# Kernel tuning notes

Measured on AMD Instinct MI355X. Metric: run time of the kernel, lower is better.

## Reference

```python
import jax, jax.numpy as jnp
import numpy as np

H = 1024
HEADS = 16
FFN = 2048
EPS = 1e-5


def _layernorm(x, g, b):
    mu = jnp.mean(x, axis=-1, keepdims=True)
    var = jnp.mean(jnp.square(x - mu), axis=-1, keepdims=True)
    return (x - mu) * jax.lax.rsqrt(var + EPS) * g + b


def setup_inputs() -> dict:
    key = jax.random.key(0)
    ks = jax.random.split(key, 8)
    N, L = 4, 1024
    s = 1.0 / np.sqrt(H)
    inp = {
        "src_hidden": jax.random.normal(ks[0], (N, L, H), dtype=jnp.float32),
        "src_mask": jnp.ones((N, L), dtype=jnp.int32),
        "Wq": jax.random.normal(ks[1], (H, H), dtype=jnp.float32) * s,
        "bq": jnp.zeros((H,), jnp.float32),
        "Wk": jax.random.normal(ks[2], (H, H), dtype=jnp.float32) * s,
        "bk": jnp.zeros((H,), jnp.float32),
        "Wv": jax.random.normal(ks[3], (H, H), dtype=jnp.float32) * s,
        "bv": jnp.zeros((H,), jnp.float32),
        "Wo": jax.random.normal(ks[4], (H, H), dtype=jnp.float32) * s,
        "bo": jnp.zeros((H,), jnp.float32),
        "ln1_g": jnp.ones((H,), jnp.float32),
        "ln1_b": jnp.zeros((H,), jnp.float32),
        "W1": jax.random.normal(ks[5], (H, FFN), dtype=jnp.float32) * s,
        "b1": jnp.zeros((FFN,), jnp.float32),
        "W2": jax.random.normal(ks[6], (FFN, H), dtype=jnp.float32) * (1.0 / np.sqrt(FFN)),
        "b2": jnp.zeros((H,), jnp.float32),
        "ln2_g": jnp.ones((H,), jnp.float32),
        "ln2_b": jnp.zeros((H,), jnp.float32),
    }
    return inp


def reference(src_hidden, src_mask, Wq, bq, Wk, bk, Wv, bv, Wo, bo,
              ln1_g, ln1_b, W1, b1, W2, b2, ln2_g, ln2_b):
    N, L, _ = src_hidden.shape
    d = H // HEADS
    scale = 1.0 / np.sqrt(H)  # applied to BOTH Q and K, as in the original
    # NOTE: head split is a plain reshape (view), faithful to the original code
    Q = ((src_hidden @ Wq + bq).reshape(N, HEADS, L, d)) * scale
    K = ((src_hidden @ Wk + bk).reshape(N, HEADS, L, d)) * scale
    V = (src_hidden @ Wv + bv).reshape(N, HEADS, L, d)
    sims = jnp.einsum('nhid,nhjd->nhij', Q, K)  # (N, heads, L, L)
    mask = src_mask[:, None, None, :]  # (N,1,1,L) broadcasts over heads and query dim
    sims = jnp.where(mask == 0, -jnp.inf, sims)
    attn = jax.nn.softmax(sims, axis=-1)
    ctx = jnp.einsum('nhij,nhjd->nhid', attn, V)
    concats = ctx.reshape(N, L, H)
    hid = concats @ Wo + bo
    x1 = _layernorm(hid, ln1_g, ln1_b) + hid
    ffn = jax.nn.relu(x1 @ W1 + b1) @ W2 + b2  # dropout is identity in eval
    out = _layernorm(ffn, ln2_g, ln2_b) + ffn
    return (out, src_mask)
```

## Files before the change

### kernel.cpp

```cpp
#include <hip/hip_runtime.h>
#include <math.h>

#define H 1024
#define HEADS 16
#define DH 64
#define FFN_DIM 2048
#define EPS 1e-5f
#define NB 4
#define LL 1024
#define M_ROWS 4096

typedef __attribute__((ext_vector_type(8))) short bf16x8;
typedef __attribute__((ext_vector_type(4))) float f32x4;

__device__ __forceinline__ ushort f2bf(float x) {
    union { float f; unsigned u; } c; c.f = x;
    unsigned u = c.u;
    u += 0x7FFFu + ((u >> 16) & 1u);
    return (ushort)(u >> 16);
}

__device__ __forceinline__ unsigned pack2bf(float a, float b) {
    union { float f; unsigned u; } ca, cb; ca.f = a; cb.f = b;
    const unsigned ua = ca.u + 0x8000u;
    const unsigned ub = cb.u + 0x8000u;
    return (ua >> 16) | (ub & 0xFFFF0000u);
}

#define GLL(gp, lp)                                                         \
    __builtin_amdgcn_global_load_lds(                                       \
        (const __attribute__((address_space(1))) void*)(gp),                \
        (__attribute__((address_space(3))) void*)(lp), 16, 0, 0)

#define WAITV4() asm volatile("s_waitcnt vmcnt(4)" ::: "memory")
#define WAITV2() asm volatile("s_waitcnt vmcnt(2)" ::: "memory")
#define WAITV0() asm volatile("s_waitcnt vmcnt(0)" ::: "memory")
#define BAR() __builtin_amdgcn_s_barrier()

__global__ __launch_bounds__(512, 8)
void gemm_bf16(const ushort* __restrict__ A, const ushort* __restrict__ Bt,
               const float* __restrict__ bias, float* __restrict__ Cf0,
               float* __restrict__ Cf1, ushort* __restrict__ Cb,
               int M, int N, int K, int relu, int qkv)
{
    __shared__ ushort As[2][128 * 32];
    __shared__ ushort Bs[2][128 * 32];
    const int tid = threadIdx.x;
    const int l = tid & 63, w = tid >> 6;
    const int wr = w >> 2, wc = w & 3;
    const int g = l >> 4, c0 = l & 15;
    const int brow = blockIdx.y * 128, bcol = blockIdx.x * 128;
    const int z = blockIdx.z;
    const int Ksub = K / gridDim.z;
    const int NS = Ksub >> 5;

    const ushort* Abase = A + (size_t)brow * K + (size_t)z * Ksub;
    const ushort* Bbase = Bt + (size_t)bcol * K + (size_t)z * Ksub;

    f32x4 acc[4][2];
    #pragma unroll
    for (int mi = 0; mi < 4; ++mi)
        #pragma unroll
        for (int ni = 0; ni < 2; ++ni)
            acc[mi][ni] = (f32x4)0.0f;

    auto stage = [&](int buf, int k0) {
        const int row = tid >> 2, cp = tid & 3;
        const int c = cp ^ ((row >> 1) & 3);
        const ushort* ga = Abase + (size_t)row * K + k0 + c * 8;
        const ushort* gb = Bbase + (size_t)row * K + k0 + c * 8;
        ushort* la = As[buf] + (size_t)w * 512;
        ushort* lb = Bs[buf] + (size_t)w * 512;
        GLL(ga, la);
        GLL(gb, lb);
    };

    stage(0, 0);
    int cur = 0;
    for (int t = 0; t < NS; ++t) {
        if (t + 1 < NS) { stage(cur ^ 1, (t + 1) << 5); WAITV2(); }
        else            { WAITV0(); }
        BAR();

        bf16x8 af[4], bf[2];
        #pragma unroll
        for (int mi = 0; mi < 4; ++mi) {
            const int row = wr * 64 + mi * 16 + c0;
            const int cc = g ^ ((row >> 1) & 3);
            af[mi] = *(const bf16x8*)&As[cur][row * 32 + cc * 8];
        }
        #pragma unroll
        for (int ni = 0; ni < 2; ++ni) {
            const int row = wc * 32 + ni * 16 + c0;
            const int cc = g ^ ((row >> 1) & 3);
            bf[ni] = *(const bf16x8*)&Bs[cur][row * 32 + cc * 8];
        }
        __builtin_amdgcn_s_setprio(1);
        #pragma unroll
        for (int mi = 0; mi < 4; ++mi)
            #pragma unroll
            for (int ni = 0; ni < 2; ++ni)
                acc[mi][ni] = __builtin_amdgcn_mfma_f32_16x16x32_bf16(
                    af[mi], bf[ni], acc[mi][ni], 0, 0, 0);
        __builtin_amdgcn_s_setprio(0);
        BAR();
        cur ^= 1;
    }

    float* Cf = (z == 0) ? Cf0 : Cf1;
    const int colg0 = bcol + wc * 32 + c0;
    const int rbase = brow + wr * 64 + (g << 2);
    const int seg   = qkv ? (bcol >> 10) : 0;
    const int Nw    = qkv ? 1024 : N;
    ushort* outb    = qkv ? (Cb + (size_t)seg * 4194304u) : Cb;
    #pragma unroll
    for (int ni = 0; ni < 2; ++ni) {
        const int colg = colg0 + ni * 16;
        const int colw = qkv ? (colg & 1023) : colg;
        const float bv = (z == 0) ? bias[colg] : 0.0f;
        #pragma unroll
        for (int mi = 0; mi < 4; ++mi) {
            #pragma unroll
            for (int j = 0; j < 4; ++j) {
                float v = acc[mi][ni][j] + bv;
                if (relu) v = fmaxf(v, 0.0f);
                const size_t off = (size_t)(rbase + mi * 16 + j) * Nw + colw;
                if (Cf) Cf[off] = v;
                if (Cb) outb[off] = f2bf(v);
            }
        }
    }
}

__global__ __launch_bounds__(256)
void transpose_qkvo(const float* __restrict__ Wq, const float* __restrict__ Wk,
                    const float* __restrict__ Wv, const float* __restrict__ Wo,
                    ushort* __restrict__ Dq, ushort* __restrict__ Dk,
                    ushort* __restrict__ Dv, ushort* __restrict__ Do_)
{
    const float* W; ushort* D; float sc;
    switch (blockIdx.z) {
        case 0:  W = Wq; D = Dq;  sc = 0.03125f; break;
        case 1:  W = Wk; D = Dk;  sc = 0.03125f; break;
        case 2:  W = Wv; D = Dv;  sc = 1.0f;     break;
        default: W = Wo; D = Do_; sc = 1.0f;     break;
    }
    __shared__ float t[32][33];
    const int n0 = blockIdx.x * 32, k0 = blockIdx.y * 32;
    const int tx = threadIdx.x & 31, ty = threadIdx.x >> 5;
    #pragma unroll
    for (int r = 0; r < 4; ++r)
        t[ty + r * 8][tx] = W[(size_t)(k0 + ty + r * 8) * H + n0 + tx];
    __syncthreads();
    #pragma unroll
    for (int r = 0; r < 4; ++r)
        D[(size_t)(n0 + ty + r * 8) * H + k0 + tx] =
            f2bf(t[tx][ty + r * 8] * sc);
}

__global__ __launch_bounds__(256)
void transpose_to_bf16(const float* __restrict__ W, ushort* __restrict__ Wt,
                       int K, int N, float scale)
{
    __shared__ float t[32][33];
    const int n0 = blockIdx.x * 32, k0 = blockIdx.y * 32;
    const int tx = threadIdx.x & 31, ty = threadIdx.x >> 5;
    #pragma unroll
    for (int r = 0; r < 4; ++r)
        t[ty + r * 8][tx] = W[(size_t)(k0 + ty + r * 8) * N + n0 + tx];
    __syncthreads();
    #pragma unroll
    for (int r = 0; r < 4; ++r)
        Wt[(size_t)(n0 + ty + r * 8) * K + k0 + tx] =
            f2bf(t[tx][ty + r * 8] * scale);
}

__global__ __launch_bounds__(256)
void transpose_v(const ushort* __restrict__ V, ushort* __restrict__ Vt)
{
    const int nh = blockIdx.y, jt = blockIdx.x;
    const size_t base = (size_t)nh << 16;
    __shared__ ushort t[64][68];
    const int tid = threadIdx.x;
    #pragma unroll
    for (int pass = 0; pass < 4; ++pass) {
        const int j = pass * 16 + (tid >> 4);
        const int d0 = (tid & 15) * 4;
        ushort4 v = *(const ushort4*)&V[base + (size_t)(jt * 64 + j) * 64 + d0];
        t[d0 + 0][j] = v.x; t[d0 + 1][j] = v.y;
        t[d0 + 2][j] = v.z; t[d0 + 3][j] = v.w;
    }
    __syncthreads();
    #pragma unroll
    for (int pass = 0; pass < 4; ++pass) {
        const int d = pass * 16 + (tid >> 4);
        const int j0 = (tid & 15) * 4;
        ushort4 o;
        o.x = t[d][j0 + 0]; o.y = t[d][j0 + 1];
        o.z = t[d][j0 + 2]; o.w = t[d][j0 + 3];
        *(ushort4*)&Vt[base + (size_t)d * 1024 + jt * 64 + j0] = o;
    }
}

__global__ __launch_bounds__(256)
void f32_to_bf16(const float* __restrict__ in, ushort* __restrict__ out, int n4)
{
    const int i = blockIdx.x * blockDim.x + threadIdx.x;
    if (i < n4) {
        float4 v = *reinterpret_cast<const float4*>(&in[i * 4]);
        ushort4 o;
        o.x = f2bf(v.x); o.y = f2bf(v.y); o.z = f2bf(v.z); o.w = f2bf(v.w);
        *reinterpret_cast<ushort4*>(&out[i * 4]) = o;
    }
}

__global__ void build_bias_qkv(const float* __restrict__ bq,
                               const float* __restrict__ bk,
                               const float* __restrict__ bv,
                               float* __restrict__ out)
{
    const int i = blockIdx.x * 256 + threadIdx.x;
    if (i >= 3072) return;
    float v;
    if (i < 1024) v = bq[i] * 0.03125f;
    else if (i < 2048) v = bk[i - 1024] * 0.03125f;
    else v = bv[i - 2048];
    out[i] = v;
}

__global__ void mask_flags(const int* __restrict__ mask, int* __restrict__ fl)
{
    const int t = threadIdx.x;
    if (t < NB * 16) {
        const int n = t >> 4, tile = t & 15;
        int any = 0;
        for (int j = 0; j < 64; ++j)
            any |= (mask[n * LL + tile * 64 + j] == 0);
        fl[t] = any;
    }
}

__global__ __launch_bounds__(256)
void attn_mfma(const ushort* __restrict__ Q, const ushort* __restrict__ K,
               const ushort* __restrict__ Vt, const int* __restrict__ mask,
               const int* __restrict__ mflags, ushort* __restrict__ ctx)
{
    const int nh = blockIdx.y;
    const int n  = nh >> 4;
    const int qb = blockIdx.x;
    const size_t hb = (size_t)nh << 16;
    const ushort* Qh = Q + hb;
    const ushort* Kh = K + hb;
    const ushort* Vh = Vt + hb;
    ushort* Ch = ctx + hb;

    __shared__ ushort Ks[2][64 * 64];
    __shared__ ushort Vs[2][64 * 64];
    __shared__ ushort Ps[4][16 * 64];

    const int tid = threadIdx.x;
    const int l = tid & 63, w = tid >> 6;
    const int g = l >> 4, c0 = l & 15;
    const int fsw = (c0 & 7) << 1;

    unsigned fbits = 0;
    #pragma unroll
    for (int tt = 0; tt < 16; ++tt)
        fbits |= (unsigned)(mflags[n * 16 + tt] != 0) << tt;

    const ushort* qrow = Qh + (size_t)(qb * 64 + w * 16 + c0) * 64;
    const bf16x8 qf0 = *(const bf16x8*)(qrow + g * 8);
    const bf16x8 qf1 = *(const bf16x8*)(qrow + 32 + g * 8);

    f32x4 Oacc[4];
    #pragma unroll
    for (int nd = 0; nd < 4; ++nd) Oacc[nd] = (f32x4)0.0f;
    float lp = 0.0f;

    auto stage = [&](int buf, int t) {
        #pragma unroll
        for (int i = 0; i < 2; ++i) {
            const int slot = i * 256 + tid;
            const int r = slot >> 3, p = slot & 7;
            const int c = p ^ (r & 7);
            const ushort* gk = Kh + (size_t)(t * 64 + r) * 64 + c * 8;
            const ushort* gv = Vh + (size_t)r * 1024 + t * 64 + c * 8;
            ushort* lk = Ks[buf] + (size_t)(i * 256 + w * 64) * 8;
            ushort* lv = Vs[buf] + (size_t)(i * 256 + w * 64) * 8;
            GLL(gk, lk);
            GLL(gv, lv);
        }
    };

    stage(0, 0);
    int cur = 0;
    for (int t = 0; t < 16; ++t) {
        if (t < 15) { stage(cur ^ 1, t + 1); WAITV4(); }
        else        { WAITV0(); }
        BAR();

        f32x4 s[4];
        #pragma unroll
        for (int nb = 0; nb < 4; ++nb) {
            s[nb] = (f32x4)0.0f;
            const int row = nb * 16 + c0;
            const int cc0 = g ^ (row & 7);
            const int cc1 = (4 + g) ^ (row & 7);
            bf16x8 kf0 = *(const bf16x8*)&Ks[cur][row * 64 + cc0 * 8];
            bf16x8 kf1 = *(const bf16x8*)&Ks[cur][row * 64 + cc1 * 8];
            __builtin_amdgcn_s_setprio(1);
            s[nb] = __builtin_amdgcn_mfma_f32_16x16x32_bf16(kf0, qf0, s[nb], 0, 0, 0);
            s[nb] = __builtin_amdgcn_mfma_f32_16x16x32_bf16(kf1, qf1, s[nb], 0, 0, 0);
            __builtin_amdgcn_s_setprio(0);
        }
        if (fbits >> t & 1) {
            #pragma unroll
            for (int nb = 0; nb < 4; ++nb)
                #pragma unroll
                for (int jr = 0; jr < 4; ++jr) {
                    const int key = 16 * nb + 4 * g + jr;
                    if (mask[n * LL + t * 64 + key] == 0)
                        s[nb][jr] = -INFINITY;
                }
        }
        #pragma unroll
        for (int nb = 0; nb < 4; ++nb)
            #pragma unroll
            for (int jr = 0; jr < 4; ++jr) {
                const float pv = __expf(s[nb][jr]);
                s[nb][jr] = pv;
                lp += pv;
            }

        ushort* Pw = Ps[w];
        #pragma unroll
        for (int nb = 0; nb < 4; ++nb) {
            const int gi = (4 * nb + g) ^ fsw;
            uint2 pk;
            pk.x = pack2bf(s[nb][0], s[nb][1]);
            pk.y = pack2bf(s[nb][2], s[nb][3]);
            *(uint2*)&Pw[c0 * 64 + gi * 4] = pk;
        }
        const bf16x8 pa0 = *(const bf16x8*)&Pw[c0 * 64 + ((2 * g) ^ fsw) * 4];
        const bf16x8 pa1 = *(const bf16x8*)&Pw[c0 * 64 + ((8 + 2 * g) ^ fsw) * 4];
        #pragma unroll
        for (int nd = 0; nd < 4; ++nd) {
            const int row = nd * 16 + c0;
            const int cc0 = g ^ (row & 7);
            const int cc1 = (4 + g) ^ (row & 7);
            bf16x8 vf0 = *(const bf16x8*)&Vs[cur][row * 64 + cc0 * 8];
            bf16x8 vf1 = *(const bf16x8*)&Vs[cur][row * 64 + cc1 * 8];
            __builtin_amdgcn_s_setprio(1);
            Oacc[nd] = __builtin_amdgcn_mfma_f32_16x16x32_bf16(pa0, vf0, Oacc[nd], 0, 0, 0);
            Oacc[nd] = __builtin_amdgcn_mfma_f32_16x16x32_bf16(pa1, vf1, Oacc[nd], 0, 0, 0);
            __builtin_amdgcn_s_setprio(0);
        }
        BAR();
        cur ^= 1;
    }

    float v = lp;
    v += __shfl_xor(v, 16, 64);
    v += __shfl_xor(v, 32, 64);
    float invq[4];
    #pragma unroll
    for (int jr = 0; jr < 4; ++jr) {
        const int src = 20 * g + jr;
        invq[jr] = 1.0f / __shfl(v, src, 64);
    }
    #pragma unroll
    for (int nd = 0; nd < 4; ++nd) {
        #pragma unroll
        for (int jr = 0; jr < 4; ++jr) {
            const int row = qb * 64 + w * 16 + 4 * g + jr;
            Ch[(size_t)row * 64 + nd * 16 + c0] = f2bf(Oacc[nd][jr] * invq[jr]);
        }
    }
}

__global__ __launch_bounds__(256)
void ln_residual(const float* __restrict__ X, const float* __restrict__ X2,
                 const float* __restrict__ g, const float* __restrict__ b,
                 float* __restrict__ outf, ushort* __restrict__ outb)
{
    const int row = blockIdx.x;
    const int tid = threadIdx.x;
    float4 xv = *reinterpret_cast<const float4*>(&X[(size_t)row * H + tid * 4]);
    if (X2) {
        float4 yv = *reinterpret_cast<const float4*>(&X2[(size_t)row * H + tid * 4]);
        xv.x += yv.x; xv.y += yv.y; xv.z += yv.z; xv.w += yv.w;
    }
    float s = xv.x + xv.y + xv.z + xv.w;
    __shared__ float red[8];
    const int lane = tid & 63, wave = tid >> 6;
    #pragma unroll
    for (int off = 32; off > 0; off >>= 1) s += __shfl_down(s, off);
    if (lane == 0) red[wave] = s;
    __syncthreads();
    if (tid == 0)
        red[0] = (red[0] + red[1] + red[2] + red[3]) * (1.0f / H);
    __syncthreads();
    const float mu = red[0];
    const float d0 = xv.x - mu, d1 = xv.y - mu, d2 = xv.z - mu, d3 = xv.w - mu;
    float s2 = d0 * d0 + d1 * d1 + d2 * d2 + d3 * d3;
    #pragma unroll
    for (int off = 32; off > 0; off >>= 1) s2 += __shfl_down(s2, off);
    if (lane == 0) red[4 + wave] = s2;
    __syncthreads();
    if (tid == 0) {
        const float var = (red[4] + red[5] + red[6] + red[7]) * (1.0f / H);
        red[4] = rsqrtf(var + EPS);
    }
    __syncthreads();
    const float rstd = red[4];
    float4 gv = *reinterpret_cast<const float4*>(&g[tid * 4]);
    float4 bv = *reinterpret_cast<const float4*>(&b[tid * 4]);
    float4 ov;
    ov.x = d0 * rstd * gv.x + bv.x + xv.x;
    ov.y = d1 * rstd * gv.y + bv.y + xv.y;
    ov.z = d2 * rstd * gv.z + bv.z + xv.z;
    ov.w = d3 * rstd * gv.w + bv.w + xv.w;
    if (outf)
        *reinterpret_cast<float4*>(&outf[(size_t)row * H + tid * 4]) = ov;
    if (outb) {
        ushort4 ob;
        ob.x = f2bf(ov.x); ob.y = f2bf(ov.y);
        ob.z = f2bf(ov.z); ob.w = f2bf(ov.w);
        *reinterpret_cast<ushort4*>(&outb[(size_t)row * H + tid * 4]) = ob;
    }
}

__global__ void mask_to_float(const int* __restrict__ m, float* __restrict__ o,
                              int n)
{
    const int i = blockIdx.x * blockDim.x + threadIdx.x;
    if (i < n) o[i] = (float)m[i];
}

extern "C" void kernel_launch(void* const* d_in, const int* in_sizes, int n_in,
                              void* d_out, int out_size, void* d_ws, size_t ws_size,
                              hipStream_t stream)
{
    const float* X    = (const float*)d_in[0];
    const int*   mask = (const int*)d_in[1];
    const float* Wq   = (const float*)d_in[2];
    const float* bq   = (const float*)d_in[3];
    const float* Wk   = (const float*)d_in[4];
    const float* bk   = (const float*)d_in[5];
    const float* Wv   = (const float*)d_in[6];
    const float* bv   = (const float*)d_in[7];
    const float* Wo   = (const float*)d_in[8];
    const float* bo   = (const float*)d_in[9];
    const float* g1   = (const float*)d_in[10];
    const float* bln1 = (const float*)d_in[11];
    const float* W1   = (const float*)d_in[12];
    const float* b1   = (const float*)d_in[13];
    const float* W2   = (const float*)d_in[14];
    const float* b2   = (const float*)d_in[15];
    const float* g2   = (const float*)d_in[16];
    const float* bln2 = (const float*)d_in[17];

    char* wsb = (char*)d_ws;
    const size_t MB = 1u << 20;
    ushort* Qb16 = (ushort*)(wsb);
    ushort* Vb16 = (ushort*)(wsb + 16 * MB);
    ushort* Xb   = (ushort*)(wsb + 24 * MB);
    ushort* ctxb = (ushort*)(wsb + 24 * MB);
    ushort* Vtb  = (ushort*)(wsb + 32 * MB);
    ushort* Wqkvt = (ushort*)(wsb + 40 * MB);
    ushort* Wot   = (ushort*)(wsb + 46 * MB);
    ushort* W1t   = (ushort*)(wsb + 40 * MB);
    ushort* W2t   = (ushort*)(wsb + 44 * MB);
    float*  biasqkv = (float*)(wsb + 48 * MB);
    int*    mfl     = (int*)(wsb + 48 * MB + 16384);
    float*  P1      = (float*)(wsb + 48 * MB);
    ushort* Fb      = (ushort*)(wsb + 48 * MB);
    float*  P0  = (float*)(wsb);
    ushort* x1b = (ushort*)(wsb + 16 * MB);
    float*  Q0  = (float*)(wsb);
    float*  Q1  = (float*)(wsb + 24 * MB);

    dim3 blk(256), gblk(512);

    f32_to_bf16<<<dim3(M_ROWS * H / 4 / 256), blk, 0, stream>>>(X, Xb, M_ROWS * H / 4);
    transpose_qkvo<<<dim3(32, 32, 4), blk, 0, stream>>>(
        Wq, Wk, Wv, Wo, Wqkvt, Wqkvt + 1024 * 1024, Wqkvt + 2048 * 1024, Wot);
    build_bias_qkv<<<dim3(12), blk, 0, stream>>>(bq, bk, bv, biasqkv);
    mask_flags<<<dim3(1), dim3(64), 0, stream>>>(mask, mfl);

    gemm_bf16<<<dim3(24, 32, 1), gblk, 0, stream>>>(
        Xb, Wqkvt, biasqkv, nullptr, nullptr, Qb16, M_ROWS, 3072, H, 0, 1);
    transpose_v<<<dim3(16, NB * HEADS), blk, 0, stream>>>(Vb16, Vtb);

    attn_mfma<<<dim3(16, NB * HEADS), blk, 0, stream>>>(
        Qb16, Qb16 + 4194304u, Vtb, mask, mfl, ctxb);

    gemm_bf16<<<dim3(8, 32, 2), gblk, 0, stream>>>(
        ctxb, Wot, bo, P0, P1, nullptr, M_ROWS, H, H, 0, 0);
    ln_residual<<<dim3(M_ROWS), blk, 0, stream>>>(P0, P1, g1, bln1, nullptr, x1b);

    transpose_to_bf16<<<dim3(FFN_DIM / 32, H / 32), blk, 0, stream>>>(W1, W1t, H, FFN_DIM, 1.0f);
    transpose_to_bf16<<<dim3(H / 32, FFN_DIM / 32), blk, 0, stream>>>(W2, W2t, FFN_DIM, H, 1.0f);

    gemm_bf16<<<dim3(16, 32, 1), gblk, 0, stream>>>(
        x1b, W1t, b1, nullptr, nullptr, Fb, M_ROWS, FFN_DIM, H, 1, 0);
    gemm_bf16<<<dim3(8, 32, 2), gblk, 0, stream>>>(
        Fb, W2t, b2, Q0, Q1, nullptr, M_ROWS, H, FFN_DIM, 0, 0);

    ln_residual<<<dim3(M_ROWS), blk, 0, stream>>>(Q0, Q1, g2, bln2, (float*)d_out, nullptr);

    mask_to_float<<<dim3((NB * LL + 255) / 256), blk, 0, stream>>>(
        mask, (float*)d_out + (size_t)M_ROWS * H, NB * LL);
}
```

Before: 197.6 us.

## Restructure GEMM to intra-block split-K with 64-deep tiles and fuse prep kernels

The GEMM now stages 64-wide K slices and splits K between two halves of the block's eight waves. Each wave computes a 64x64 output tile, and the halves' partial sums are reduced through LDS before the epilogue. This replaces the grid-level split-K with its two float partial outputs, so the LN kernels read a single buffer. All preprocessing kernels (X conversion, weight transposes, bias build, mask flags, mask output) are merged into one launch to cut launch count. In exchange the GEMM has higher register and LDS use (occupancy hint lowered to 4) and an extra LDS reduction step.

```diff
diff --git a/kernel.cpp b/kernel.cpp
--- a/kernel.cpp
+++ b/kernel.cpp
@@ -33,73 +33,75 @@
         (__attribute__((address_space(3))) void*)(lp), 16, 0, 0)
 
 #define WAITV4() asm volatile("s_waitcnt vmcnt(4)" ::: "memory")
-#define WAITV2() asm volatile("s_waitcnt vmcnt(2)" ::: "memory")
 #define WAITV0() asm volatile("s_waitcnt vmcnt(0)" ::: "memory")
 #define BAR() __builtin_amdgcn_s_barrier()
 
-__global__ __launch_bounds__(512, 8)
+__global__ __launch_bounds__(512, 4)
 void gemm_bf16(const ushort* __restrict__ A, const ushort* __restrict__ Bt,
-               const float* __restrict__ bias, float* __restrict__ Cf0,
-               float* __restrict__ Cf1, ushort* __restrict__ Cb,
-               int M, int N, int K, int relu, int qkv)
+               const float* __restrict__ bias, float* __restrict__ Cf,
+               ushort* __restrict__ Cb, int M, int N, int K,
+               int relu, int qkv)
 {
-    __shared__ ushort As[2][128 * 32];
-    __shared__ ushort Bs[2][128 * 32];
+    __shared__ ushort As[2][128 * 64];
+    __shared__ ushort Bs[2][128 * 64];
     const int tid = threadIdx.x;
     const int l = tid & 63, w = tid >> 6;
-    const int wr = w >> 2, wc = w & 3;
+    const int h  = w >> 2;
+    const int wr = (w >> 1) & 1, wc = w & 1;
     const int g = l >> 4, c0 = l & 15;
     const int brow = blockIdx.y * 128, bcol = blockIdx.x * 128;
-    const int z = blockIdx.z;
-    const int Ksub = K / gridDim.z;
-    const int NS = Ksub >> 5;
-
-    const ushort* Abase = A + (size_t)brow * K + (size_t)z * Ksub;
-    const ushort* Bbase = Bt + (size_t)bcol * K + (size_t)z * Ksub;
-
-    f32x4 acc[4][2];
+    const int NS = K >> 6;
+
+    const ushort* Abase = A + (size_t)brow * K;
+    const ushort* Bbase = Bt + (size_t)bcol * K;
+
+    f32x4 acc[4][4];
     #pragma unroll
     for (int mi = 0; mi < 4; ++mi)
         #pragma unroll
-        for (int ni = 0; ni < 2; ++ni)
+        for (int ni = 0; ni < 4; ++ni)
             acc[mi][ni] = (f32x4)0.0f;
 
     auto stage = [&](int buf, int k0) {
-        const int row = tid >> 2, cp = tid & 3;
-        const int c = cp ^ ((row >> 1) & 3);
-        const ushort* ga = Abase + (size_t)row * K + k0 + c * 8;
-        const ushort* gb = Bbase + (size_t)row * K + k0 + c * 8;
-        ushort* la = As[buf] + (size_t)w * 512;
-        ushort* lb = Bs[buf] + (size_t)w * 512;
-        GLL(ga, la);
-        GLL(gb, lb);
+        #pragma unroll
+        for (int i = 0; i < 2; ++i) {
+            const int f = i * 512 + tid;
+            const int row = f >> 3, p = f & 7;
+            const int c = p ^ (row & 7);
+            const ushort* ga = Abase + (size_t)row * K + k0 + c * 8;
+            const ushort* gb = Bbase + (size_t)row * K + k0 + c * 8;
+            ushort* la = As[buf] + (size_t)(i * 512 + w * 64) * 8;
+            ushort* lb = Bs[buf] + (size_t)(i * 512 + w * 64) * 8;
+            GLL(ga, la);
+            GLL(gb, lb);
+        }
     };
 
     stage(0, 0);
     int cur = 0;
     for (int t = 0; t < NS; ++t) {
-        if (t + 1 < NS) { stage(cur ^ 1, (t + 1) << 5); WAITV2(); }
+        if (t + 1 < NS) { stage(cur ^ 1, (t + 1) << 6); WAITV4(); }
         else            { WAITV0(); }
         BAR();
 
-        bf16x8 af[4], bf[2];
+        bf16x8 af[4], bf[4];
         #pragma unroll
         for (int mi = 0; mi < 4; ++mi) {
             const int row = wr * 64 + mi * 16 + c0;
-            const int cc = g ^ ((row >> 1) & 3);
-            af[mi] = *(const bf16x8*)&As[cur][row * 32 + cc * 8];
-        }
-        #pragma unroll
-        for (int ni = 0; ni < 2; ++ni) {
-            const int row = wc * 32 + ni * 16 + c0;
-            const int cc = g ^ ((row >> 1) & 3);
-            bf[ni] = *(const bf16x8*)&Bs[cur][row * 32 + cc * 8];
+            const int cc = (h * 4 + g) ^ (row & 7);
+            af[mi] = *(const bf16x8*)&As[cur][row * 64 + cc * 8];
+        }
+        #pragma unroll
+        for (int ni = 0; ni < 4; ++ni) {
+            const int row = wc * 64 + ni * 16 + c0;
+            const int cc = (h * 4 + g) ^ (row & 7);
+            bf[ni] = *(const bf16x8*)&Bs[cur][row * 64 + cc * 8];
         }
         __builtin_amdgcn_s_setprio(1);
         #pragma unroll
         for (int mi = 0; mi < 4; ++mi)
             #pragma unroll
-            for (int ni = 0; ni < 2; ++ni)
+            for (int ni = 0; ni < 4; ++ni)
                 acc[mi][ni] = __builtin_amdgcn_mfma_f32_16x16x32_bf16(
                     af[mi], bf[ni], acc[mi][ni], 0, 0, 0);
         __builtin_amdgcn_s_setprio(0);
@@ -107,17 +109,41 @@
         cur ^= 1;
     }
 
-    float* Cf = (z == 0) ? Cf0 : Cf1;
-    const int colg0 = bcol + wc * 32 + c0;
+    if (h == 1) {
+        const int u = w - 4;
+        f32x4* zone = (u & 2) ? (f32x4*)Bs : (f32x4*)As;
+        const int uu = u & 1;
+        #pragma unroll
+        for (int mi = 0; mi < 4; ++mi)
+            #pragma unroll
+            for (int ni = 0; ni < 4; ++ni)
+                zone[(size_t)((uu * 16 + mi * 4 + ni) * 64 + l)] = acc[mi][ni];
+    }
+    __syncthreads();
+    if (h == 1) return;
+
+    {
+        f32x4* zone = (w & 2) ? (f32x4*)Bs : (f32x4*)As;
+        const int uu = w & 1;
+        #pragma unroll
+        for (int mi = 0; mi < 4; ++mi)
+            #pragma unroll
+            for (int ni = 0; ni < 4; ++ni) {
+                f32x4 p = zone[(size_t)((uu * 16 + mi * 4 + ni) * 64 + l)];
+                acc[mi][ni] += p;
+            }
+    }
+
+    const int colg0 = bcol + wc * 64 + c0;
     const int rbase = brow + wr * 64 + (g << 2);
     const int seg   = qkv ? (bcol >> 10) : 0;
     const int Nw    = qkv ? 1024 : N;
     ushort* outb    = qkv ? (Cb + (size_t)seg * 4194304u) : Cb;
     #pragma unroll
-    for (int ni = 0; ni < 2; ++ni) {
+    for (int ni = 0; ni < 4; ++ni) {
         const int colg = colg0 + ni * 16;
         const int colw = qkv ? (colg & 1023) : colg;
-        const float bv = (z == 0) ? bias[colg] : 0.0f;
+        const float bv = bias[colg];
         #pragma unroll
         for (int mi = 0; mi < 4; ++mi) {
             #pragma unroll
@@ -133,46 +159,87 @@
 }
 
 __global__ __launch_bounds__(256)
-void transpose_qkvo(const float* __restrict__ Wq, const float* __restrict__ Wk,
-                    const float* __restrict__ Wv, const float* __restrict__ Wo,
-                    ushort* __restrict__ Dq, ushort* __restrict__ Dk,
-                    ushort* __restrict__ Dv, ushort* __restrict__ Do_)
+void prep(const float* __restrict__ X, ushort* __restrict__ Xb,
+          const float* __restrict__ Wq, const float* __restrict__ Wk,
+          const float* __restrict__ Wv, const float* __restrict__ Wo,
+          const float* __restrict__ W1, const float* __restrict__ W2,
+          ushort* __restrict__ Wqkvt, ushort* __restrict__ Wot,
+          ushort* __restrict__ W1t, ushort* __restrict__ W2t,
+          const float* __restrict__ bq, const float* __restrict__ bk,
+          const float* __restrict__ bv, float* __restrict__ biasqkv,
+          const int* __restrict__ mask, int* __restrict__ mfl,
+          float* __restrict__ maskout)
 {
-    const float* W; ushort* D; float sc;
-    switch (blockIdx.z) {
-        case 0:  W = Wq; D = Dq;  sc = 0.03125f; break;
-        case 1:  W = Wk; D = Dk;  sc = 0.03125f; break;
-        case 2:  W = Wv; D = Dv;  sc = 1.0f;     break;
-        default: W = Wo; D = Do_; sc = 1.0f;     break;
-    }
-    __shared__ float t[32][33];
-    const int n0 = blockIdx.x * 32, k0 = blockIdx.y * 32;
-    const int tx = threadIdx.x & 31, ty = threadIdx.x >> 5;
-    #pragma unroll
-    for (int r = 0; r < 4; ++r)
-        t[ty + r * 8][tx] = W[(size_t)(k0 + ty + r * 8) * H + n0 + tx];
-    __syncthreads();
-    #pragma unroll
-    for (int r = 0; r < 4; ++r)
-        D[(size_t)(n0 + ty + r * 8) * H + k0 + tx] =
-            f2bf(t[tx][ty + r * 8] * sc);
-}
-
-__global__ __launch_bounds__(256)
-void transpose_to_bf16(const float* __restrict__ W, ushort* __restrict__ Wt,
-                       int K, int N, float scale)
-{
-    __shared__ float t[32][33];
-    const int n0 = blockIdx.x * 32, k0 = blockIdx.y * 32;
-    const int tx = threadIdx.x & 31, ty = threadIdx.x >> 5;
-    #pragma unroll
-    for (int r = 0; r < 4; ++r)
-        t[ty + r * 8][tx] = W[(size_t)(k0 + ty + r * 8) * N + n0 + tx];
-    __syncthreads();
-    #pragma unroll
-    for (int r = 0; r < 4; ++r)
-        Wt[(size_t)(n0 + ty + r * 8) * K + k0 + tx] =
-            f2bf(t[tx][ty + r * 8] * scale);
+    const int b = blockIdx.x;
+    const int tid = threadIdx.x;
+
+    if (b < 4096) {
+        const int i = b * 256 + tid;
+        float4 v = *reinterpret_cast<const float4*>(&X[(size_t)i * 4]);
+        ushort4 o;
+        o.x = f2bf(v.x); o.y = f2bf(v.y); o.z = f2bf(v.z); o.w = f2bf(v.w);
+        *reinterpret_cast<ushort4*>(&Xb[(size_t)i * 4]) = o;
+        return;
+    }
+    int r = b - 4096;
+    const float* W = nullptr; ushort* D = nullptr;
+    int K = H, N = H; float sc = 1.0f; int blin = 0;
+    if (r < 4096) {
+        const int which = r >> 10;
+        blin = r & 1023;
+        switch (which) {
+            case 0: W = Wq; D = Wqkvt;               sc = 0.03125f; break;
+            case 1: W = Wk; D = Wqkvt + 1024 * 1024; sc = 0.03125f; break;
+            case 2: W = Wv; D = Wqkvt + 2048 * 1024; sc = 1.0f;     break;
+            default: W = Wo; D = Wot;                sc = 1.0f;     break;
+        }
+    } else if (r < 4096 + 2048) {
+        W = W1; D = W1t; K = H; N = FFN_DIM; blin = r - 4096;
+    } else if (r < 4096 + 4096) {
+        W = W2; D = W2t; K = FFN_DIM; N = H; blin = r - 4096 - 2048;
+    }
+    if (W) {
+        __shared__ float t[32][33];
+        const int nbx = N >> 5;
+        const int bx = blin % nbx, by = blin / nbx;
+        const int n0 = bx * 32, k0 = by * 32;
+        const int tx = tid & 31, ty = tid >> 5;
+        #pragma unroll
+        for (int rr = 0; rr < 4; ++rr)
+            t[ty + rr * 8][tx] = W[(size_t)(k0 + ty + rr * 8) * N + n0 + tx];
+        __syncthreads();
+        #pragma unroll
+        for (int rr = 0; rr < 4; ++rr)
+            D[(size_t)(n0 + ty + rr * 8) * K + k0 + tx] =
+                f2bf(t[tx][ty + rr * 8] * sc);
+        return;
+    }
+    r -= 8192;
+    if (r < 12) {
+        const int i = r * 256 + tid;
+        if (i < 3072) {
+            float v;
+            if (i < 1024) v = bq[i] * 0.03125f;
+            else if (i < 2048) v = bk[i - 1024] * 0.03125f;
+            else v = bv[i - 2048];
+            biasqkv[i] = v;
+        }
+        return;
+    }
+    if (r == 12) {
+        if (tid < NB * 16) {
+            const int n = tid >> 4, tile = tid & 15;
+            int any = 0;
+            for (int j = 0; j < 64; ++j)
+                any |= (mask[n * LL + tile * 64 + j] == 0);
+            mfl[tid] = any;
+        }
+        return;
+    }
+    {
+        const int i = (r - 13) * 256 + tid;
+        if (i < NB * LL) maskout[i] = (float)mask[i];
+    }
 }
 
 __global__ __launch_bounds__(256)
@@ -199,44 +266,6 @@
         o.x = t[d][j0 + 0]; o.y = t[d][j0 + 1];
         o.z = t[d][j0 + 2]; o.w = t[d][j0 + 3];
         *(ushort4*)&Vt[base + (size_t)d * 1024 + jt * 64 + j0] = o;
-    }
-}
-
-__global__ __launch_bounds__(256)
-void f32_to_bf16(const float* __restrict__ in, ushort* __restrict__ out, int n4)
-{
-    const int i = blockIdx.x * blockDim.x + threadIdx.x;
-    if (i < n4) {
-        float4 v = *reinterpret_cast<const float4*>(&in[i * 4]);
-        ushort4 o;
-        o.x = f2bf(v.x); o.y = f2bf(v.y); o.z = f2bf(v.z); o.w = f2bf(v.w);
-        *reinterpret_cast<ushort4*>(&out[i * 4]) = o;
-    }
-}
-
-__global__ void build_bias_qkv(const float* __restrict__ bq,
-                               const float* __restrict__ bk,
-                               const float* __restrict__ bv,
-                               float* __restrict__ out)
-{
-    const int i = blockIdx.x * 256 + threadIdx.x;
-    if (i >= 3072) return;
-    float v;
-    if (i < 1024) v = bq[i] * 0.03125f;
-    else if (i < 2048) v = bk[i - 1024] * 0.03125f;
-    else v = bv[i - 2048];
-    out[i] = v;
-}
-
-__global__ void mask_flags(const int* __restrict__ mask, int* __restrict__ fl)
-{
-    const int t = threadIdx.x;
-    if (t < NB * 16) {
-        const int n = t >> 4, tile = t & 15;
-        int any = 0;
-        for (int j = 0; j < 64; ++j)
-            any |= (mask[n * LL + tile * 64 + j] == 0);
-        fl[t] = any;
     }
 }
 
@@ -428,13 +457,6 @@
         ob.z = f2bf(ov.z); ob.w = f2bf(ov.w);
         *reinterpret_cast<ushort4*>(&outb[(size_t)row * H + tid * 4]) = ob;
     }
-}
-
-__global__ void mask_to_float(const int* __restrict__ m, float* __restrict__ o,
-                              int n)
-{
-    const int i = blockIdx.x * blockDim.x + threadIdx.x;
-    if (i < n) o[i] = (float)m[i];
 }
 
 extern "C" void kernel_launch(void* const* d_in, const int* in_sizes, int n_in,
@@ -467,48 +489,41 @@
     ushort* Xb   = (ushort*)(wsb + 24 * MB);
     ushort* ctxb = (ushort*)(wsb + 24 * MB);
     ushort* Vtb  = (ushort*)(wsb + 32 * MB);
+    ushort* x1b  = (ushort*)(wsb + 32 * MB);
     ushort* Wqkvt = (ushort*)(wsb + 40 * MB);
     ushort* Wot   = (ushort*)(wsb + 46 * MB);
-    ushort* W1t   = (ushort*)(wsb + 40 * MB);
-    ushort* W2t   = (ushort*)(wsb + 44 * MB);
-    float*  biasqkv = (float*)(wsb + 48 * MB);
-    int*    mfl     = (int*)(wsb + 48 * MB + 16384);
-    float*  P1      = (float*)(wsb + 48 * MB);
-    ushort* Fb      = (ushort*)(wsb + 48 * MB);
-    float*  P0  = (float*)(wsb);
-    ushort* x1b = (ushort*)(wsb + 16 * MB);
-    float*  Q0  = (float*)(wsb);
-    float*  Q1  = (float*)(wsb + 24 * MB);
+    ushort* W1t   = (ushort*)(wsb + 48 * MB);
+    ushort* W2t   = (ushort*)(wsb + 52 * MB);
+    float*  biasqkv = (float*)(wsb + 56 * MB);
+    int*    mfl     = (int*)(wsb + 56 * MB + 16384);
+    float*  hid = (float*)(wsb);
+    ushort* Fb  = (ushort*)(wsb + 16 * MB);
+    float*  ffn = (float*)(wsb);
 
     dim3 blk(256), gblk(512);
 
-    f32_to_bf16<<<dim3(M_ROWS * H / 4 / 256), blk, 0, stream>>>(X, Xb, M_ROWS * H / 4);
-    transpose_qkvo<<<dim3(32, 32, 4), blk, 0, stream>>>(
-        Wq, Wk, Wv, Wo, Wqkvt, Wqkvt + 1024 * 1024, Wqkvt + 2048 * 1024, Wot);
-    build_bias_qkv<<<dim3(12), blk, 0, stream>>>(bq, bk, bv, biasqkv);
-    mask_flags<<<dim3(1), dim3(64), 0, stream>>>(mask, mfl);
-
-    gemm_bf16<<<dim3(24, 32, 1), gblk, 0, stream>>>(
-        Xb, Wqkvt, biasqkv, nullptr, nullptr, Qb16, M_ROWS, 3072, H, 0, 1);
+    prep<<<dim3(4096 + 4096 + 2048 + 2048 + 12 + 1 + 16), blk, 0, stream>>>(
+        X, Xb, Wq, Wk, Wv, Wo, W1, W2, Wqkvt, Wot, W1t, W2t,
+        bq, bk, bv, biasqkv, mask, mfl,
+        (float*)d_out + (size_t)M_ROWS * H);
+
+    gemm_bf16<<<dim3(24, 32), gblk, 0, stream>>>(
+        Xb, Wqkvt, biasqkv, nullptr, Qb16, M_ROWS, 3072, H, 0, 1);
     transpose_v<<<dim3(16, NB * HEADS), blk, 0, stream>>>(Vb16, Vtb);
 
     attn_mfma<<<dim3(16, NB * HEADS), blk, 0, stream>>>(
         Qb16, Qb16 + 4194304u, Vtb, mask, mfl, ctxb);
 
-    gemm_bf16<<<dim3(8, 32, 2), gblk, 0, stream>>>(
-        ctxb, Wot, bo, P0, P1, nullptr, M_ROWS, H, H, 0, 0);
-    ln_residual<<<dim3(M_ROWS), blk, 0, stream>>>(P0, P1, g1, bln1, nullptr, x1b);
-
-    transpose_to_bf16<<<dim3(FFN_DIM / 32, H / 32), blk, 0, stream>>>(W1, W1t, H, FFN_DIM, 1.0f);
-    transpose_to_bf16<<<dim3(H / 32, FFN_DIM / 32), blk, 0, stream>>>(W2, W2t, FFN_DIM, H, 1.0f);
-
-    gemm_bf16<<<dim3(16, 32, 1), gblk, 0, stream>>>(
-        x1b, W1t, b1, nullptr, nullptr, Fb, M_ROWS, FFN_DIM, H, 1, 0);
-    gemm_bf16<<<dim3(8, 32, 2), gblk, 0, stream>>>(
-        Fb, W2t, b2, Q0, Q1, nullptr, M_ROWS, H, FFN_DIM, 0, 0);
-
-    ln_residual<<<dim3(M_ROWS), blk, 0, stream>>>(Q0, Q1, g2, bln2, (float*)d_out, nullptr);
-
-    mask_to_float<<<dim3((NB * LL + 255) / 256), blk, 0, stream>>>(
-        mask, (float*)d_out + (size_t)M_ROWS * H, NB * LL);
-}
+    gemm_bf16<<<dim3(8, 32), gblk, 0, stream>>>(
+        ctxb, Wot, bo, hid, nullptr, M_ROWS, H, H, 0, 0);
+    ln_residual<<<dim3(M_ROWS), blk, 0, stream>>>(hid, nullptr, g1, bln1,
+                                                  nullptr, x1b);
+
+    gemm_bf16<<<dim3(16, 32), gblk, 0, stream>>>(
+        x1b, W1t, b1, nullptr, Fb, M_ROWS, FFN_DIM, H, 1, 0);
+    gemm_bf16<<<dim3(8, 32), gblk, 0, stream>>>(
+        Fb, W2t, b2, ffn, nullptr, M_ROWS, H, FFN_DIM, 0, 0);
+
+    ln_residual<<<dim3(M_ROWS), blk, 0, stream>>>(ffn, nullptr, g2, bln2,
+                                                  (float*)d_out, nullptr);
+}
```

New measurement: 199.8 us. No clear change (+1.1%).
